# Kernel optimization log

Measured on AMD Instinct MI355X. Metric: run time of the kernel, lower is better.

The kernel has to match this reference:

```python
import jax, jax.numpy as jnp
from jax import lax
import numpy as np

B, C_IN, C_OUT, T, N, E = 4, 32, 32, 48, 2000, 16000


def _tconv(x, w, b):
    # Conv2d with kernel (3,1), padding (1,0): temporal conv over T, per-node.
    y = lax.conv_general_dilated(x, w, window_strides=(1, 1),
                                 padding=((1, 1), (0, 0)),
                                 dimension_numbers=('NCHW', 'OIHW', 'NCHW'))
    return y + b[None, :, None, None]


def setup_inputs() -> dict:
    key = jax.random.key(0)
    ks = jax.random.split(key, 8)
    x = jax.random.normal(ks[0], (B, C_IN, T, N), dtype=jnp.float32)
    edge_index = jax.random.randint(ks[1], (2, E), 0, N, dtype=jnp.int64)
    w1 = jax.random.normal(ks[2], (C_OUT, C_IN, 3, 1), dtype=jnp.float32) * 0.05
    b1 = jnp.zeros((C_OUT,), dtype=jnp.float32)
    gcn_w = jax.random.normal(ks[3], (C_OUT, C_OUT), dtype=jnp.float32) * 0.05
    gcn_b = jnp.zeros((C_OUT,), dtype=jnp.float32)
    w2 = jax.random.normal(ks[4], (C_OUT, C_OUT, 3, 1), dtype=jnp.float32) * 0.05
    b2 = jnp.zeros((C_OUT,), dtype=jnp.float32)
    return {"x": x, "edge_index": edge_index, "w1": w1, "b1": b1,
            "gcn_w": gcn_w, "gcn_b": gcn_b, "w2": w2, "b2": b2}


def reference(x, edge_index, w1, b1, gcn_w, gcn_b, w2, b2):
    # temporal conv 1 + relu
    h = jax.nn.relu(_tconv(x, w1, b1))          # [B, C, T, N]
    Bs, C, Ts, Ns = h.shape
    # replicate-graph GCN: same edge_index for all B*T graphs
    xf = h.transpose(0, 2, 3, 1).reshape(Bs * Ts, Ns, C)   # [BT, N, C]
    xw = xf @ gcn_w                                        # linear transform first
    src, dst = edge_index[0], edge_index[1]
    # GCN symmetric normalization with self-loops: deg = 1 + in-degree
    deg = jnp.zeros((Ns,), xw.dtype).at[dst].add(1.0) + 1.0
    dinv = lax.rsqrt(deg)
    wedge = dinv[src] * dinv[dst]                           # [E]

    def aggregate(g):  # g: [N, C] for one graph
        return jnp.zeros((Ns, C), g.dtype).at[dst].add(g[src] * wedge[:, None])

    agg = jax.vmap(aggregate)(xw)                           # [BT, N, C]
    out = agg + (1.0 / deg)[None, :, None] * xw + gcn_b     # self-loop term + bias
    out = out.reshape(Bs, Ts, Ns, C).transpose(0, 3, 1, 2)  # [B, C, T, N]
    # temporal conv 2
    return _tconv(out, w2, b2)
```

## Files before the change

kernel.cpp:

```cpp
#include <hip/hip_runtime.h>

#define BB 4
#define CIN 32
#define COUT 32
#define TT 48
#define NN 2000
#define EE 16000
#define BT (BB*TT)
#define PADCOL 24576


__global__ __launch_bounds__(256) void k_zero(int* __restrict__ col,
                                              float* __restrict__ wedge) {
    int i = blockIdx.x * 256 + threadIdx.x;
    if (i < PADCOL) { col[i] = 0; wedge[i] = 0.f; }
}


__global__ __launch_bounds__(1024) void k_build(
        const int* __restrict__ ei,
        const float* __restrict__ w1, const float* __restrict__ gw,
        const float* __restrict__ gb, const float* __restrict__ w2,
        const float* __restrict__ cb2,
        int* __restrict__ rowptr, float* __restrict__ dinv2,
        float* __restrict__ dinvg, int* __restrict__ fillptr,
        float* __restrict__ w1t, float* __restrict__ w2c,
        float* __restrict__ biasE) {
    __shared__ int   cnt[2048];
    __shared__ int   buf[2048];
    __shared__ float sw2t[3072];
    __shared__ float sgw[1024];
    __shared__ float sbk[96];
    int t = threadIdx.x;

    for (int i = t; i < 3072; i += 1024) {
        int c = i & 31, r = i >> 5;
        int co = r & 31, k = r >> 5;
        sw2t[i] = w2[c * 96 + co * 3 + k];
        w1t[i]  = w1[c * 96 + co * 3 + k];
    }
    sgw[t] = gw[t];
    cnt[t] = 0; cnt[t + 1024] = 0;
    __syncthreads();

    for (int e = t; e < EE; e += 1024) atomicAdd(&cnt[ei[EE + e]], 1);
    __syncthreads();

    for (int i = t; i < 2048; i += 1024)
        buf[i] = (i < NN) ? ((cnt[i] + 3) & ~3) : 0;
    __syncthreads();
    for (int s = 1; s < 2048; s <<= 1) {
        int i0 = t, i1 = t + 1024;
        int a0 = buf[i0] + ((i0 >= s) ? buf[i0 - s] : 0);
        int a1 = buf[i1] + ((i1 >= s) ? buf[i1 - s] : 0);
        __syncthreads();
        buf[i0] = a0; buf[i1] = a1;
        __syncthreads();
    }

    for (int i = t; i < 2048; i += 1024) {
        if (i < NN) {
            rowptr[i + 1] = buf[i];
            float deg = (float)(cnt[i] + 1);
            dinvg[i] = rsqrtf(deg);
            dinv2[i] = 1.0f / deg;
            fillptr[i] = buf[i] - ((cnt[i] + 3) & ~3);
        }
    }
    if (t == 0) rowptr[0] = 0;


    for (int i = t; i < 3072; i += 1024) {
        int c = i & 31, r = i >> 5;
        int cm = r & 31, k = r >> 5;
        float acc = 0.f;
#pragma unroll
        for (int co = 0; co < 32; co++)
            acc += sgw[cm * 32 + co] * sw2t[(k * 32 + co) * 32 + c];
        w2c[i] = acc;
    }
    for (int i = t; i < 96; i += 1024) {
        int k = i >> 5, c = i & 31;
        float acc = 0.f;
#pragma unroll
        for (int co = 0; co < 32; co++)
            acc += gb[co] * sw2t[(k * 32 + co) * 32 + c];
        sbk[i] = acc;
    }
    __syncthreads();
    for (int i = t; i < 96; i += 1024) {
        int cls = i >> 5, c = i & 31;
        float v = cb2[c] + sbk[32 + c];
        if (cls != 0) v += sbk[c];
        if (cls != 2) v += sbk[64 + c];
        biasE[i] = v;
    }
}


__global__ void k_fill(const int* __restrict__ ei, int* __restrict__ fillptr,
                       const float* __restrict__ dinvg,
                       int* __restrict__ col, float* __restrict__ wedge) {
    int e = blockIdx.x * blockDim.x + threadIdx.x;
    if (e < EE) {
        int s = ei[e], d = ei[EE + e];
        int pos = atomicAdd(fillptr + d, 1);
        col[pos]   = s;
        wedge[pos] = dinvg[s] * dinvg[d];
    }
}


__global__ __launch_bounds__(256) void k_conv1(const float* __restrict__ x,
                                               const float* __restrict__ w1t,
                                               const float* __restrict__ b1,
                                               float* __restrict__ hbuf) {
    int bid = blockIdx.x;
    int xcd = bid & 7;
    int i   = bid >> 3;
    int nch = i & 7;
    int r   = i >> 3;
    int tloc = r % 6, b = r / 6;
    int t = xcd * 6 + tloc;
    int n = nch * 256 + threadIdx.x;
    if (n >= NN) return;
    int g = b * TT + t;
    int gb = g >> 3, gsub = g & 7;

    float ha[COUT];
#pragma unroll
    for (int c = 0; c < COUT; c++) ha[c] = b1[c];

    const float* xbase = x + ((size_t)b * CIN * TT) * NN + n;
    bool hasL = (t > 0), hasR = (t < TT - 1);
    const float* pL = xbase + (size_t)(hasL ? t - 1 : 0) * NN;
    const float* pM = xbase + (size_t)t * NN;
    const float* pR = xbase + (size_t)(hasR ? t + 1 : 0) * NN;

    float xa[CIN], xm[CIN];
#pragma unroll
    for (int ci = 0; ci < CIN; ci++) xa[ci] = pL[(size_t)ci * TT * NN];
#pragma unroll
    for (int ci = 0; ci < CIN; ci++) xm[ci] = pM[(size_t)ci * TT * NN];
    __builtin_amdgcn_sched_barrier(0);

    if (hasL) {
        const float* wp = w1t;
#pragma unroll
        for (int ci = 0; ci < CIN; ci++) {
#pragma unroll
            for (int c = 0; c < COUT; c++) ha[c] += xa[ci] * wp[ci * COUT + c];
        }
    }
    __builtin_amdgcn_sched_barrier(0);

#pragma unroll
    for (int ci = 0; ci < CIN; ci++) xa[ci] = pR[(size_t)ci * TT * NN];
    __builtin_amdgcn_sched_barrier(0);

    {
        const float* wp = w1t + 1024;
#pragma unroll
        for (int ci = 0; ci < CIN; ci++) {
#pragma unroll
            for (int c = 0; c < COUT; c++) ha[c] += xm[ci] * wp[ci * COUT + c];
        }
    }
    __builtin_amdgcn_sched_barrier(0);

    if (hasR) {
        const float* wp = w1t + 2048;
#pragma unroll
        for (int ci = 0; ci < CIN; ci++) {
#pragma unroll
            for (int c = 0; c < COUT; c++) ha[c] += xa[ci] * wp[ci * COUT + c];
        }
    }

    float4* pa = (float4*)(hbuf + (((size_t)gb * NN + n) * 8 + gsub) * 32);
#pragma unroll
    for (int q = 0; q < 8; q++)
        pa[q] = make_float4(fmaxf(ha[4*q], 0.f), fmaxf(ha[4*q+1], 0.f),
                            fmaxf(ha[4*q+2], 0.f), fmaxf(ha[4*q+3], 0.f));
}


__global__ __launch_bounds__(256) void k_agg(const float* __restrict__ hbuf,
                                             const int* __restrict__ rowptr,
                                             const int* __restrict__ col,
                                             const float* __restrict__ wedge,
                                             const float* __restrict__ dinv2,
                                             float* __restrict__ gbuf) {
    int bid = blockIdx.x;
    int xcd = bid & 7;
    int q   = bid >> 3;
    int gbr = q / 500;
    int nch = q % 500;
    int gb  = gbr * 8 + xcd;
    int wid  = threadIdx.x >> 6;
    int lane = threadIdx.x & 63;
    int gsub = lane >> 3;
    int cq   = lane & 7;
    int n    = nch * 4 + wid;

    const float* xg = hbuf + (size_t)gb * NN * 256;
    size_t loff = (size_t)gsub * 32 + cq * 4;

    float4 self = *(const float4*)(xg + (size_t)n * 256 + loff);
    float dv = dinv2[n];
    float4 acc = make_float4(dv * self.x, dv * self.y, dv * self.z, dv * self.w);

    int j  = rowptr[n];
    int je = rowptr[n + 1];
    for (; j < je; j += 4) {
        int4   cc = *(const int4*)(col + j);
        float4 ww = *(const float4*)(wedge + j);
        float4 v0 = *(const float4*)(xg + (size_t)cc.x * 256 + loff);
        float4 v1 = *(const float4*)(xg + (size_t)cc.y * 256 + loff);
        float4 v2 = *(const float4*)(xg + (size_t)cc.z * 256 + loff);
        float4 v3 = *(const float4*)(xg + (size_t)cc.w * 256 + loff);
        acc.x += ww.x*v0.x + ww.y*v1.x + ww.z*v2.x + ww.w*v3.x;
        acc.y += ww.x*v0.y + ww.y*v1.y + ww.z*v2.y + ww.w*v3.y;
        acc.z += ww.x*v0.z + ww.y*v1.z + ww.z*v2.z + ww.w*v3.z;
        acc.w += ww.x*v0.w + ww.y*v1.w + ww.z*v2.w + ww.w*v3.w;
    }

    int g = gb * 8 + gsub;
    *(float4*)(gbuf + ((size_t)g * NN + n) * 32 + cq * 4) = acc;
}


#define LD32(GV, GP) { \
    _Pragma("unroll") \
    for (int q_ = 0; q_ < 8; q_++) { \
        float4 v_ = (GP)[q_]; \
        GV[4*q_] = v_.x; GV[4*q_+1] = v_.y; GV[4*q_+2] = v_.z; GV[4*q_+3] = v_.w; } }

#define FMA32(ACC, GV, WP) { \
    _Pragma("unroll") \
    for (int cm_ = 0; cm_ < 32; cm_++) { \
        float g_ = GV[cm_]; \
        _Pragma("unroll") \
        for (int c_ = 0; c_ < 32; c_++) ACC[c_] += g_ * (WP)[cm_ * 32 + c_]; } }

__global__ __launch_bounds__(256) void k_conv2(const float* __restrict__ gbuf,
                                               const float* __restrict__ w2c,
                                               const float* __restrict__ biasE,
                                               float* __restrict__ out) {
    int bid  = blockIdx.x;
    int xcd  = bid & 7;
    int slot = bid >> 3;
    int grp  = xcd * 24 + (slot >> 3);
    int nch  = slot & 7;
    int b = grp / TT;
    int t = grp % TT;
    int n = nch * 256 + threadIdx.x;
    if (n >= NN) return;

    bool hasL = (t > 0), hasR = (t < TT - 1);
    const float4* pL = (const float4*)(gbuf + (((size_t)(b * TT + (hasL ? t - 1 : 0))) * NN + n) * CIN);
    const float4* pM = (const float4*)(gbuf + (((size_t)(b * TT + t)) * NN + n) * CIN);
    const float4* pR = (const float4*)(gbuf + (((size_t)(b * TT + (hasR ? t + 1 : 0))) * NN + n) * CIN);

    float o[COUT];
#pragma unroll
    for (int c = 0; c < COUT; c++) o[c] = 0.f;

    float ga[CIN], gm[CIN];
    LD32(ga, pL);
    LD32(gm, pM);
    __builtin_amdgcn_sched_barrier(0);

    if (hasL) { FMA32(o, ga, w2c); }
    __builtin_amdgcn_sched_barrier(0);

    LD32(ga, pR);
    __builtin_amdgcn_sched_barrier(0);

    FMA32(o, gm, w2c + 1024);
    __builtin_amdgcn_sched_barrier(0);

    if (hasR) { FMA32(o, ga, w2c + 2048); }

    int cls = (t == 0) ? 0 : ((t == TT - 1) ? 2 : 1);
    const float* bp = biasE + cls * 32;
#pragma unroll
    for (int c = 0; c < COUT; c++)
        out[(((size_t)b * COUT + c) * TT + t) * NN + n] = o[c] + bp[c];
}


extern "C" void kernel_launch(void* const* d_in, const int* in_sizes, int n_in,
                              void* d_out, int out_size, void* d_ws, size_t ws_size,
                              hipStream_t stream) {
    const float* x     = (const float*)d_in[0];
    const int*   ei    = (const int*)d_in[1];
    const float* w1    = (const float*)d_in[2];
    const float* b1    = (const float*)d_in[3];
    const float* gcn_w = (const float*)d_in[4];
    const float* gcn_b = (const float*)d_in[5];
    const float* w2    = (const float*)d_in[6];
    const float* b2    = (const float*)d_in[7];
    float* out = (float*)d_out;

    const size_t XWB = (size_t)BT * NN * COUT * sizeof(float);
    char* w = (char*)d_ws;
    float* hbuf    = (float*)w;  w += XWB;
    float* gbuf    = (float*)w;  w += XWB;
    int*   rowptr  = (int*)w;    w += 8192;
    float* dinv2   = (float*)w;  w += 8192;
    float* dinvg   = (float*)w;  w += 8192;
    int*   fillptr = (int*)w;    w += 8192;
    int*   col     = (int*)w;    w += PADCOL * sizeof(int);
    float* wedge   = (float*)w;  w += PADCOL * sizeof(float);
    float* w1t     = (float*)w;  w += 3072 * sizeof(float);
    float* w2c     = (float*)w;  w += 3072 * sizeof(float);
    float* biasE   = (float*)w;  w += 96 * sizeof(float);

    k_zero <<<dim3((PADCOL + 255) / 256), dim3(256), 0, stream>>>(col, wedge);
    k_build<<<dim3(1), dim3(1024), 0, stream>>>(ei, w1, gcn_w, gcn_b, w2, b2,
                                                rowptr, dinv2, dinvg, fillptr,
                                                w1t, w2c, biasE);
    k_fill <<<dim3((EE + 255) / 256), dim3(256), 0, stream>>>(ei, fillptr, dinvg, col, wedge);
    k_conv1<<<dim3(1536), dim3(256), 0, stream>>>(x, w1t, b1, hbuf);
    k_agg  <<<dim3(12000), dim3(256), 0, stream>>>(hbuf, rowptr, col, wedge, dinv2, gbuf);
    k_conv2<<<dim3(1536), dim3(256), 0, stream>>>(gbuf, w2c, biasE, out);
}
```

Baseline: 233.9 us.

## Split single-block graph build into parallel count, weight-prep, and scan kernels

The single 1024-thread build kernel, which did the edge degree counting, the weight folding and the prefix scan all in one block, is split into separate kernels. Degree counting now runs across many blocks with global atomics. Weight transposition and the folding of the GCN weights into conv2 run in a 13-block kernel. The remaining single block only loads the counts and scans them. This spreads the serial preprocessing over more compute units, at the cost of two extra kernel launches and global rather than shared atomics.

```diff
diff --git a/kernel.cpp b/kernel.cpp
--- a/kernel.cpp
+++ b/kernel.cpp
@@ -11,39 +11,65 @@
 
 
 __global__ __launch_bounds__(256) void k_zero(int* __restrict__ col,
-                                              float* __restrict__ wedge) {
+                                              float* __restrict__ wedge,
+                                              int* __restrict__ gcnt) {
     int i = blockIdx.x * 256 + threadIdx.x;
     if (i < PADCOL) { col[i] = 0; wedge[i] = 0.f; }
-}
-
-
-__global__ __launch_bounds__(1024) void k_build(
-        const int* __restrict__ ei,
+    if (i < 2048)   gcnt[i] = 0;
+}
+
+
+__global__ __launch_bounds__(256) void k_count(const int* __restrict__ ei,
+                                               int* __restrict__ gcnt) {
+    int e = blockIdx.x * 256 + threadIdx.x;
+    if (e < EE) atomicAdd(&gcnt[ei[EE + e]], 1);
+}
+
+
+__global__ __launch_bounds__(256) void k_wprep(
         const float* __restrict__ w1, const float* __restrict__ gw,
         const float* __restrict__ gb, const float* __restrict__ w2,
         const float* __restrict__ cb2,
-        int* __restrict__ rowptr, float* __restrict__ dinv2,
-        float* __restrict__ dinvg, int* __restrict__ fillptr,
         float* __restrict__ w1t, float* __restrict__ w2c,
         float* __restrict__ biasE) {
-    __shared__ int   cnt[2048];
-    __shared__ int   buf[2048];
-    __shared__ float sw2t[3072];
-    __shared__ float sgw[1024];
-    __shared__ float sbk[96];
-    int t = threadIdx.x;
-
-    for (int i = t; i < 3072; i += 1024) {
+    int i = blockIdx.x * 256 + threadIdx.x;
+    if (i < 3072) {
         int c = i & 31, r = i >> 5;
         int co = r & 31, k = r >> 5;
-        sw2t[i] = w2[c * 96 + co * 3 + k];
-        w1t[i]  = w1[c * 96 + co * 3 + k];
-    }
-    sgw[t] = gw[t];
-    cnt[t] = 0; cnt[t + 1024] = 0;
-    __syncthreads();
-
-    for (int e = t; e < EE; e += 1024) atomicAdd(&cnt[ei[EE + e]], 1);
+        w1t[i] = w1[c * 96 + co * 3 + k];
+        float acc = 0.f;
+#pragma unroll
+        for (int q = 0; q < 32; q++)
+            acc += gw[co * 32 + q] * w2[c * 96 + q * 3 + k];
+        w2c[i] = acc;
+    } else if (i < 3168) {
+        int j = i - 3072;
+        int cls = j >> 5, c = j & 31;
+        float bk0 = 0.f, bk1 = 0.f, bk2 = 0.f;
+#pragma unroll
+        for (int co = 0; co < 32; co++) {
+            float g = gb[co];
+            bk0 += g * w2[c * 96 + co * 3 + 0];
+            bk1 += g * w2[c * 96 + co * 3 + 1];
+            bk2 += g * w2[c * 96 + co * 3 + 2];
+        }
+        float v = cb2[c] + bk1;
+        if (cls != 0) v += bk0;
+        if (cls != 2) v += bk2;
+        biasE[j] = v;
+    }
+}
+
+
+__global__ __launch_bounds__(1024) void k_build(
+        const int* __restrict__ gcnt,
+        int* __restrict__ rowptr, float* __restrict__ dinv2,
+        float* __restrict__ dinvg, int* __restrict__ fillptr) {
+    __shared__ int cnt[2048];
+    __shared__ int buf[2048];
+    int t = threadIdx.x;
+
+    cnt[t] = gcnt[t]; cnt[t + 1024] = gcnt[t + 1024];
     __syncthreads();
 
     for (int i = t; i < 2048; i += 1024)
@@ -68,33 +94,6 @@
         }
     }
     if (t == 0) rowptr[0] = 0;
-
-
-    for (int i = t; i < 3072; i += 1024) {
-        int c = i & 31, r = i >> 5;
-        int cm = r & 31, k = r >> 5;
-        float acc = 0.f;
-#pragma unroll
-        for (int co = 0; co < 32; co++)
-            acc += sgw[cm * 32 + co] * sw2t[(k * 32 + co) * 32 + c];
-        w2c[i] = acc;
-    }
-    for (int i = t; i < 96; i += 1024) {
-        int k = i >> 5, c = i & 31;
-        float acc = 0.f;
-#pragma unroll
-        for (int co = 0; co < 32; co++)
-            acc += gb[co] * sw2t[(k * 32 + co) * 32 + c];
-        sbk[i] = acc;
-    }
-    __syncthreads();
-    for (int i = t; i < 96; i += 1024) {
-        int cls = i >> 5, c = i & 31;
-        float v = cb2[c] + sbk[32 + c];
-        if (cls != 0) v += sbk[c];
-        if (cls != 2) v += sbk[64 + c];
-        biasE[i] = v;
-    }
 }
 
 
@@ -311,16 +310,18 @@
     float* dinv2   = (float*)w;  w += 8192;
     float* dinvg   = (float*)w;  w += 8192;
     int*   fillptr = (int*)w;    w += 8192;
+    int*   gcnt    = (int*)w;    w += 8192;
     int*   col     = (int*)w;    w += PADCOL * sizeof(int);
     float* wedge   = (float*)w;  w += PADCOL * sizeof(float);
     float* w1t     = (float*)w;  w += 3072 * sizeof(float);
     float* w2c     = (float*)w;  w += 3072 * sizeof(float);
     float* biasE   = (float*)w;  w += 96 * sizeof(float);
 
-    k_zero <<<dim3((PADCOL + 255) / 256), dim3(256), 0, stream>>>(col, wedge);
-    k_build<<<dim3(1), dim3(1024), 0, stream>>>(ei, w1, gcn_w, gcn_b, w2, b2,
-                                                rowptr, dinv2, dinvg, fillptr,
+    k_zero <<<dim3((PADCOL + 255) / 256), dim3(256), 0, stream>>>(col, wedge, gcnt);
+    k_count<<<dim3((EE + 255) / 256), dim3(256), 0, stream>>>(ei, gcnt);
+    k_wprep<<<dim3(13), dim3(256), 0, stream>>>(w1, gcn_w, gcn_b, w2, b2,
                                                 w1t, w2c, biasE);
+    k_build<<<dim3(1), dim3(1024), 0, stream>>>(gcnt, rowptr, dinv2, dinvg, fillptr);
     k_fill <<<dim3((EE + 255) / 256), dim3(256), 0, stream>>>(ei, fillptr, dinvg, col, wedge);
     k_conv1<<<dim3(1536), dim3(256), 0, stream>>>(x, w1t, b1, hbuf);
     k_agg  <<<dim3(12000), dim3(256), 0, stream>>>(hbuf, rowptr, col, wedge, dinv2, gbuf);
```

Result: no change. 232.1 us (-0.8%).
